# Kernel optimization log

Measured on AMD Instinct MI355X. Metric: run time of the kernel, lower is better.

The kernel has to match this reference:

```python
import jax, jax.numpy as jnp
import numpy as np

F = 256          # in_features
T = 8            # num_fragment_ion_types = 4 types * 2 charges
N_MONO, N_CLEAV, N_FRAG, N_OUT = 150000, 100000, 80000, 40000
D_CLEAV, D_JOIN, D_COMB = 4, 2, 4


def setup_inputs() -> dict:
    key = jax.random.key(0)
    ks = jax.random.split(key, 14)
    s = 0.05
    return {
        "feature": jax.random.normal(ks[0], (N_MONO, F), jnp.float32),
        "Wg_lost": jax.random.normal(ks[1], (F, 1), jnp.float32) * s,
        "Wg_ret": jax.random.normal(ks[2], (F, 1), jnp.float32) * s,
        "W_ih": jax.random.normal(ks[3], (4 * F, 2 * F), jnp.float32) * s,
        "W_hh": jax.random.normal(ks[4], (4 * F, F), jnp.float32) * s,
        "b_ih": jax.random.normal(ks[5], (4 * F,), jnp.float32) * s,
        "b_hh": jax.random.normal(ks[6], (4 * F,), jnp.float32) * s,
        "Wg_frag": jax.random.normal(ks[7], (F, 1), jnp.float32) * s,
        "W_out": jax.random.normal(ks[8], (F, T), jnp.float32) * s,
        "b_out": jnp.zeros((T,), jnp.float32),
        "lost_src": jax.random.randint(ks[9], (N_CLEAV, D_CLEAV), 0, N_MONO),
        "retained_src": jax.random.randint(ks[10], (N_CLEAV, D_CLEAV), 0, N_MONO),
        "join_src": jax.random.randint(ks[11], (N_FRAG, D_JOIN), 0, N_CLEAV),
        "combine_src": jax.random.randint(ks[12], (N_OUT, D_COMB), 0, N_FRAG),
    }


def _attention_sum(h, Wg):
    # h: [N, D, F] mailbox; gate = Linear(F,1,no bias); softmax over neighbor axis
    logits = jnp.einsum('ndf,fo->ndo', h, Wg)          # [N, D, 1]
    a = jax.nn.softmax(logits, axis=1)
    return jnp.sum(a * h, axis=1)                       # [N, F]


def _lstm(x, W_ih, W_hh, b_ih, b_hh):
    # x: [N, L, I]; torch nn.LSTM gate order i,f,g,o; zero initial state
    N = x.shape[0]
    H = W_hh.shape[1]
    def step(carry, xt):
        h, c = carry
        gates = xt @ W_ih.T + h @ W_hh.T + b_ih + b_hh  # [N, 4H]
        i, f, g, o = jnp.split(gates, 4, axis=-1)
        c = jax.nn.sigmoid(f) * c + jax.nn.sigmoid(i) * jnp.tanh(g)
        h = jax.nn.sigmoid(o) * jnp.tanh(c)
        return (h, c), h
    init = (jnp.zeros((N, H), x.dtype), jnp.zeros((N, H), x.dtype))
    _, hs = jax.lax.scan(step, init, jnp.swapaxes(x, 0, 1))
    return jnp.swapaxes(hs, 0, 1)                       # [N, L, H]


def reference(feature, Wg_lost, Wg_ret, W_ih, W_hh, b_ih, b_hh,
              Wg_frag, W_out, b_out,
              lost_src, retained_src, join_src, combine_src):
    h_lost = _attention_sum(feature[lost_src], Wg_lost)        # [N_cleav, F]
    h_ret = _attention_sum(feature[retained_src], Wg_ret)      # [N_cleav, F]
    cleav = jnp.concatenate([h_lost, h_ret], axis=-1)          # [N_cleav, 2F]
    # Fragment pull over 'join' edges: LSTM over neighbor set, then attention sum
    hs = _lstm(cleav[join_src], W_ih, W_hh, b_ih, b_hh)        # [N_frag, D_join, F]
    frag = _attention_sum(hs, Wg_frag)                         # [N_frag, F]
    # Output head: Linear + ReLU
    frag_out = jax.nn.relu(frag @ W_out + b_out)               # [N_frag, T]
    # copy_u_sum over 'combine' edges: scatter-sum of src outputs to dst
    return frag_out[combine_src].sum(axis=1)                   # [N_out, T]
```

## Files before the change

kernel.cpp:

```cpp
#include <hip/hip_runtime.h>

typedef unsigned short u16;
typedef unsigned int u32;
typedef float f32x4 __attribute__((ext_vector_type(4)));
typedef __bf16 bf16x8 __attribute__((ext_vector_type(8)));

#define F 256
#define T_OUT 8
#define N_MONO 150000
#define N_CLEAV 100000
#define N_FRAG 80000
#define N_FRAG_PAD 80128
#define N_OUT 40000
#define M_CLEAV_PAD 100352

static __device__ __forceinline__ u16 f2bf(float f) {
  u32 u = __float_as_uint(f);
  u32 r = (u + 0x7FFFu + ((u >> 16) & 1u)) >> 16;
  return (u16)r;
}
static __device__ __forceinline__ float bf2f(u16 b) {
  return __uint_as_float(((u32)b) << 16);
}
static __device__ __forceinline__ float sigmoidf(float x) {
  return __frcp_rn(1.0f + __expf(-x));
}
static __device__ __forceinline__ float fast_tanh(float x) {
  return 1.0f - 2.0f * __frcp_rn(__expf(2.0f * x) + 1.0f);
}
static __device__ __forceinline__ void async_copy16(const u16* g, const u16* l) {
  __builtin_amdgcn_global_load_lds(
      (const __attribute__((address_space(1))) u32*)g,
      (__attribute__((address_space(3))) u32*)l,
      16, 0, 0);
}

__global__ __launch_bounds__(256) void prep_kernel(
    const float* __restrict__ Wih, const float* __restrict__ Whh,
    const float* __restrict__ bih, const float* __restrict__ bhh,
    u16* __restrict__ Wihb, u16* __restrict__ Whhb, float* __restrict__ bias) {
  int i = blockIdx.x * 256 + threadIdx.x;
  if (i < 1024 * 512) Wihb[i] = f2bf(Wih[i]);
  if (i < 1024 * 256) Whhb[i] = f2bf(Whh[i]);
  if (i < 1024) bias[i] = bih[i] + bhh[i];
}

__global__ __launch_bounds__(256) void feat_prep(
    const float* __restrict__ feat, const float* __restrict__ WgL,
    const float* __restrict__ WgR, u16* __restrict__ featb,
    float* __restrict__ glog) {
  int wave = threadIdx.x >> 6, lane = threadIdx.x & 63;
  int n = blockIdx.x * 4 + wave;
  if (n >= N_MONO) return;
  float4 x = *(const float4*)(feat + (size_t)n * F + lane * 4);
  u32 lo = (u32)f2bf(x.x) | ((u32)f2bf(x.y) << 16);
  u32 hi = (u32)f2bf(x.z) | ((u32)f2bf(x.w) << 16);
  *(uint2*)(featb + (size_t)n * F + lane * 4) = make_uint2(lo, hi);
  float4 wl = *(const float4*)(WgL + lane * 4);
  float4 wr = *(const float4*)(WgR + lane * 4);
  float pl = x.x * wl.x + x.y * wl.y + x.z * wl.z + x.w * wl.w;
  float pr = x.x * wr.x + x.y * wr.y + x.z * wr.z + x.w * wr.w;
#pragma unroll
  for (int off = 32; off; off >>= 1) {
    pl += __shfl_xor(pl, off);
    pr += __shfl_xor(pr, off);
  }
  if (lane == 0) {
    glog[n * 2] = pl;
    glog[n * 2 + 1] = pr;
  }
}

__global__ __launch_bounds__(256) void attn_pull2(
    const u16* __restrict__ featb, const float* __restrict__ glog,
    const int* __restrict__ lostS, const int* __restrict__ retS,
    u16* __restrict__ cleav) {
  int wave = threadIdx.x >> 6, lane = threadIdx.x & 63;
  int n0 = blockIdx.x * 8 + wave * 2;
  if (n0 >= N_CLEAV) return;
  int r[2][2][4];
#pragma unroll
  for (int c = 0; c < 2; ++c) {
    int4 rl = *(const int4*)(lostS + (n0 + c) * 4);
    int4 rr = *(const int4*)(retS + (n0 + c) * 4);
    r[c][0][0] = rl.x; r[c][0][1] = rl.y; r[c][0][2] = rl.z; r[c][0][3] = rl.w;
    r[c][1][0] = rr.x; r[c][1][1] = rr.y; r[c][1][2] = rr.z; r[c][1][3] = rr.w;
  }
  ushort4 x4[2][2][4];
  float lg[2][2][4];
#pragma unroll
  for (int c = 0; c < 2; ++c)
#pragma unroll
    for (int sg = 0; sg < 2; ++sg)
#pragma unroll
      for (int d = 0; d < 4; ++d) {
        x4[c][sg][d] = *(const ushort4*)(featb + (size_t)r[c][sg][d] * F + lane * 4);
        lg[c][sg][d] = glog[r[c][sg][d] * 2 + sg];
      }
#pragma unroll
  for (int c = 0; c < 2; ++c)
#pragma unroll
    for (int sg = 0; sg < 2; ++sg) {
      float l0 = lg[c][sg][0], l1 = lg[c][sg][1];
      float l2 = lg[c][sg][2], l3 = lg[c][sg][3];
      float mx = fmaxf(fmaxf(l0, l1), fmaxf(l2, l3));
      float e0 = __expf(l0 - mx), e1 = __expf(l1 - mx);
      float e2 = __expf(l2 - mx), e3 = __expf(l3 - mx);
      float inv = __frcp_rn(e0 + e1 + e2 + e3);
      float a[4] = {e0 * inv, e1 * inv, e2 * inv, e3 * inv};
      float acc[4] = {0.f, 0.f, 0.f, 0.f};
#pragma unroll
      for (int d = 0; d < 4; ++d) {
        const u16* xp = (const u16*)&x4[c][sg][d];
#pragma unroll
        for (int k = 0; k < 4; k++) acc[k] += a[d] * bf2f(xp[k]);
      }
      u32 lo = (u32)f2bf(acc[0]) | ((u32)f2bf(acc[1]) << 16);
      u32 hi = (u32)f2bf(acc[2]) | ((u32)f2bf(acc[3]) << 16);
      *(uint2*)(cleav + (size_t)(n0 + c) * 512 + sg * 256 + lane * 4) =
          make_uint2(lo, hi);
    }
}

__global__ __launch_bounds__(512, 2) void gemm224(
    const u16* __restrict__ A, const u16* __restrict__ Bw,
    u16* __restrict__ C, const float* __restrict__ bias,
    int nper, int mstrips_valid) {
  constexpr int K = 512, BM = 224;
  constexpr int AREG = BM * 64;
  constexpr int BSZ = AREG + 16384;
  constexpr int WMH = BM / 2;
  constexpr int IB = BM / 32;
  constexpr int IB_HI = IB - 4;
  __shared__ u16 sh[2][BSZ];
  const int flat = blockIdx.x;
  const int xcd = flat & 7;
  const int w = flat >> 3;
  const int mstrip = xcd * nper + (w >> 2);
  const int nstrip = w & 3;
  if (mstrip >= mstrips_valid) return;
  const int m0 = mstrip * BM;
  const int n0 = nstrip * 256;

  const int tid = threadIdx.x;
  const int lane = tid & 63;
  const int wave = tid >> 6;
  const int quad = lane >> 4;
  const int l16 = lane & 15;
  const int s7 = l16 & 7;
  const int wm2 = wave >> 2;
  const int wn4 = wave & 3;

  const int arow = (wm2 * WMH + l16) * 64;
  const int brow = AREG + (wn4 * 64 + l16) * 64;
  const int coff0 = (quad ^ s7) * 8;
  const int coff1 = ((4 + quad) ^ s7) * 8;

  int sr[4], sw[4], dwv[4];
#pragma unroll
  for (int r = 0; r < 4; r++) {
    int c = r * 512 + tid;
    sr[r] = c >> 3;
    sw[r] = ((c & 7) ^ ((c >> 3) & 7)) * 8;
    dwv[r] = (r * 512 + (tid & ~63)) * 8;
  }
  const u16* Abase = A + (size_t)m0 * K;
  const u16* Bbase = Bw + (size_t)n0 * K;

  auto stageA = [&](int buf, int kt, int h) {
#pragma unroll
    for (int rr = 0; rr < 2; rr++) {
      int r = 2 * h + rr;
      if (r * 512 + tid < BM * 8)
        async_copy16(Abase + (size_t)sr[r] * K + kt * 64 + sw[r], &sh[buf][dwv[r]]);
    }
  };
  auto stageB = [&](int buf, int kt, int h) {
#pragma unroll
    for (int rr = 0; rr < 2; rr++) {
      int r = 2 * h + rr;
      async_copy16(Bbase + (size_t)sr[r] * K + kt * 64 + sw[r], &sh[buf][AREG + dwv[r]]);
    }
  };

  f32x4 acc[IB][4];
#pragma unroll
  for (int i = 0; i < IB; i++)
#pragma unroll
    for (int j = 0; j < 4; j++) acc[i][j] = (f32x4){0.f, 0.f, 0.f, 0.f};

  constexpr int nK = K / 64;
  stageA(0, 0, 0); stageA(0, 0, 1); stageB(0, 0, 0); stageB(0, 0, 1);
  stageB(1, 1, 0); stageB(1, 1, 1);
  __builtin_amdgcn_s_waitcnt(0xF74);
  __builtin_amdgcn_s_barrier();

  bf16x8 a[4][2], b0[2][2], b1[2][2];
#pragma unroll
  for (int t = 0; t < nK; ++t) {
    const int bsel = t & 1;
    const u16* S = &sh[bsel][0];

#pragma unroll
    for (int i = 0; i < 4; i++) {
      a[i][0] = *(const bf16x8*)&S[arow + i * 1024 + coff0];
      a[i][1] = *(const bf16x8*)&S[arow + i * 1024 + coff1];
    }
#pragma unroll
    for (int j = 0; j < 2; j++) {
      b0[j][0] = *(const bf16x8*)&S[brow + j * 1024 + coff0];
      b0[j][1] = *(const bf16x8*)&S[brow + j * 1024 + coff1];
    }
    if (t + 1 < nK) stageA(bsel ^ 1, t + 1, 0);
    __builtin_amdgcn_s_waitcnt(0xC87F);
    __builtin_amdgcn_s_barrier();
    __builtin_amdgcn_s_waitcnt(0xC07F);
    __builtin_amdgcn_sched_barrier(0);
    __builtin_amdgcn_s_setprio(1);
#pragma unroll
    for (int i = 0; i < 4; i++)
#pragma unroll
      for (int j = 0; j < 2; j++) {
        acc[i][j] = __builtin_amdgcn_mfma_f32_16x16x32_bf16(a[i][0], b0[j][0], acc[i][j], 0, 0, 0);
        acc[i][j] = __builtin_amdgcn_mfma_f32_16x16x32_bf16(a[i][1], b0[j][1], acc[i][j], 0, 0, 0);
      }
    __builtin_amdgcn_s_setprio(0);
    __builtin_amdgcn_s_barrier();

#pragma unroll
    for (int j = 0; j < 2; j++) {
      b1[j][0] = *(const bf16x8*)&S[brow + (2 + j) * 1024 + coff0];
      b1[j][1] = *(const bf16x8*)&S[brow + (2 + j) * 1024 + coff1];
    }
    if (t + 1 < nK) stageA(bsel ^ 1, t + 1, 1);
    __builtin_amdgcn_s_barrier();
    __builtin_amdgcn_s_waitcnt(0xC07F);
    __builtin_amdgcn_sched_barrier(0);
    __builtin_amdgcn_s_setprio(1);
#pragma unroll
    for (int i = 0; i < 4; i++)
#pragma unroll
      for (int j = 0; j < 2; j++) {
        acc[i][2 + j] = __builtin_amdgcn_mfma_f32_16x16x32_bf16(a[i][0], b1[j][0], acc[i][2 + j], 0, 0, 0);
        acc[i][2 + j] = __builtin_amdgcn_mfma_f32_16x16x32_bf16(a[i][1], b1[j][1], acc[i][2 + j], 0, 0, 0);
      }
    __builtin_amdgcn_s_setprio(0);
    __builtin_amdgcn_s_barrier();

#pragma unroll
    for (int i = 0; i < IB_HI; i++) {
      a[i][0] = *(const bf16x8*)&S[arow + (4 + i) * 1024 + coff0];
      a[i][1] = *(const bf16x8*)&S[arow + (4 + i) * 1024 + coff1];
    }
    if (t + 2 < nK) stageB(bsel, t + 2, 0);
    __builtin_amdgcn_s_barrier();
    __builtin_amdgcn_s_waitcnt(0xC07F);
    __builtin_amdgcn_sched_barrier(0);
    __builtin_amdgcn_s_setprio(1);
#pragma unroll
    for (int i = 0; i < IB_HI; i++)
#pragma unroll
      for (int j = 0; j < 2; j++) {
        acc[4 + i][j] = __builtin_amdgcn_mfma_f32_16x16x32_bf16(a[i][0], b0[j][0], acc[4 + i][j], 0, 0, 0);
        acc[4 + i][j] = __builtin_amdgcn_mfma_f32_16x16x32_bf16(a[i][1], b0[j][1], acc[4 + i][j], 0, 0, 0);
      }
    __builtin_amdgcn_s_setprio(0);
    __builtin_amdgcn_s_barrier();

    if (t + 2 < nK) stageB(bsel, t + 2, 1);
    __builtin_amdgcn_s_barrier();
    __builtin_amdgcn_s_setprio(1);
#pragma unroll
    for (int i = 0; i < IB_HI; i++)
#pragma unroll
      for (int j = 0; j < 2; j++) {
        acc[4 + i][2 + j] = __builtin_amdgcn_mfma_f32_16x16x32_bf16(a[i][0], b1[j][0], acc[4 + i][2 + j], 0, 0, 0);
        acc[4 + i][2 + j] = __builtin_amdgcn_mfma_f32_16x16x32_bf16(a[i][1], b1[j][1], acc[4 + i][2 + j], 0, 0, 0);
      }
    __builtin_amdgcn_s_setprio(0);
    if (t + 2 < nK) __builtin_amdgcn_s_waitcnt(0xF74);
    else            __builtin_amdgcn_s_waitcnt(0xF70);
    __builtin_amdgcn_s_barrier();
  }

  float badd[4];
#pragma unroll
  for (int j = 0; j < 4; j++)
    badd[j] = bias[n0 + wn4 * 64 + j * 16 + l16];
#pragma unroll
  for (int i = 0; i < IB; i++) {
    const int mrow = m0 + wm2 * WMH + i * 16 + quad * 4;
#pragma unroll
    for (int j = 0; j < 4; j++) {
      const int n = n0 + wn4 * 64 + j * 16 + l16;
#pragma unroll
      for (int r = 0; r < 4; r++)
        C[(size_t)(mrow + r) * 1024 + n] = f2bf(acc[i][j][r] + badd[j]);
    }
  }
}

__global__ __launch_bounds__(256) void lstm_step1(
    const u16* __restrict__ P, const int* __restrict__ join,
    u16* __restrict__ h1, u16* __restrict__ c1) {
  int wave = threadIdx.x >> 6, lane = threadIdx.x & 63;
  int m0 = blockIdx.x * 8 + wave * 2;
  if (m0 >= N_FRAG_PAD) return;
#pragma unroll
  for (int c = 0; c < 2; ++c) {
    int m = m0 + c;
    if (m >= N_FRAG) {
      if (m < N_FRAG_PAD) {
        *(ushort4*)(h1 + (size_t)m * 256 + lane * 4) = make_ushort4(0, 0, 0, 0);
        *(ushort4*)(c1 + (size_t)m * 256 + lane * 4) = make_ushort4(0, 0, 0, 0);
      }
    }
  }
  if (m0 + 1 >= N_FRAG) return;
  int j0a = join[2 * m0];
  int j0b = join[2 * (m0 + 1)];
  const u16* rowa = P + (size_t)j0a * 1024 + lane * 4;
  const u16* rowb = P + (size_t)j0b * 1024 + lane * 4;
  ushort4 iva = *(const ushort4*)(rowa);
  ushort4 gva = *(const ushort4*)(rowa + 512);
  ushort4 ova = *(const ushort4*)(rowa + 768);
  ushort4 ivb = *(const ushort4*)(rowb);
  ushort4 gvb = *(const ushort4*)(rowb + 512);
  ushort4 ovb = *(const ushort4*)(rowb + 768);
#pragma unroll
  for (int c = 0; c < 2; ++c) {
    const u16* ivp = (const u16*)(c ? &ivb : &iva);
    const u16* gvp = (const u16*)(c ? &gvb : &gva);
    const u16* ovp = (const u16*)(c ? &ovb : &ova);
    ushort4 h4, c4;
    u16* h4p = (u16*)&h4;
    u16* c4p = (u16*)&c4;
#pragma unroll
    for (int k = 0; k < 4; k++) {
      float cc = sigmoidf(bf2f(ivp[k])) * fast_tanh(bf2f(gvp[k]));
      float hv = sigmoidf(bf2f(ovp[k])) * fast_tanh(cc);
      h4p[k] = f2bf(hv);
      c4p[k] = f2bf(cc);
    }
    *(ushort4*)(h1 + (size_t)(m0 + c) * 256 + lane * 4) = h4;
    *(ushort4*)(c1 + (size_t)(m0 + c) * 256 + lane * 4) = c4;
  }
}

__global__ __launch_bounds__(256, 3) void g2fuse(
    const u16* __restrict__ h1A, const u16* __restrict__ Whhb,
    const u16* __restrict__ P, const int* __restrict__ join,
    const u16* __restrict__ c1in, u16* __restrict__ h2s) {
  constexpr int K = 256;
  __shared__ u16 sh[6][128 * 32];
  const int b = blockIdx.x;
  const int xcd = b & 7;
  const int k = b >> 3;
  const int nstrip = k & 7;
  const int mstrip = (k >> 3) * 8 + xcd;
  if (mstrip >= 626) return;
  const int m0 = mstrip * 128;

  const int tid = threadIdx.x;
  const int lane = tid & 63;
  const int wave = tid >> 6;
  const int quad = lane >> 4;
  const int l16 = lane & 15;
  const int wm = (wave & 1) * 64;
  const int wnq = wave >> 1;
  const int wn = wnq * 64;

  int srow[2], skoff[2], ldsoff[2], brow[2];
#pragma unroll
  for (int jj = 0; jj < 2; jj++) {
    int c = jj * 256 + tid;
    int row = c >> 2;
    srow[jj] = row;
    skoff[jj] = ((c & 3) ^ ((c >> 3) & 3)) * 8;
    ldsoff[jj] = (jj * 256 + (tid & ~63)) * 8;
    brow[jj] = ((row >> 4) & 3) * 256 + nstrip * 32 + ((row >> 6) << 4) + (row & 15);
  }
  const u16* Abase = h1A + (size_t)m0 * K;

  int jrow[8];
#pragma unroll
  for (int rd = 0; rd < 8; rd++) {
    int mm = m0 + rd * 16 + (tid >> 4);
    jrow[rd] = join[2 * (mm < N_FRAG ? mm : N_FRAG - 1) + 1];
  }

  auto stage = [&](int buf, int k0) {
#pragma unroll
    for (int jj = 0; jj < 2; jj++)
      async_copy16(Abase + (size_t)srow[jj] * K + k0 + skoff[jj], &sh[buf][ldsoff[jj]]);
#pragma unroll
    for (int jj = 0; jj < 2; jj++)
      async_copy16(Whhb + (size_t)brow[jj] * K + k0 + skoff[jj], &sh[3 + buf][ldsoff[jj]]);
  };

  f32x4 acc[4][4];
#pragma unroll
  for (int i = 0; i < 4; i++)
#pragma unroll
    for (int j = 0; j < 4; j++) acc[i][j] = (f32x4){0.f, 0.f, 0.f, 0.f};

  constexpr int nK = K / 32;
  stage(0, 0);
  stage(1, 32);
#pragma unroll
  for (int t = 0; t < nK; ++t) {
    if (t < nK - 1) __builtin_amdgcn_s_waitcnt(0xF74);
    else            __builtin_amdgcn_s_waitcnt(0xF70);
    __builtin_amdgcn_s_barrier();
    if (t + 2 < nK) stage((t + 2) % 3, (t + 2) * 32);
    const int buf = t % 3;
    bf16x8 af[4], bfr[4];
#pragma unroll
    for (int i = 0; i < 4; i++) {
      int m = wm + i * 16 + l16;
      int jp = quad ^ ((m >> 1) & 3);
      af[i] = *(const bf16x8*)&sh[buf][m * 32 + jp * 8];
    }
#pragma unroll
    for (int j = 0; j < 4; j++) {
      int n = wn + j * 16 + l16;
      int jp = quad ^ ((n >> 1) & 3);
      bfr[j] = *(const bf16x8*)&sh[3 + buf][n * 32 + jp * 8];
    }
#pragma unroll
    for (int i = 0; i < 4; i++)
#pragma unroll
      for (int j = 0; j < 4; j++)
        acc[i][j] = __builtin_amdgcn_mfma_f32_16x16x32_bf16(af[i], bfr[j], acc[i][j], 0, 0, 0);
  }

  __builtin_amdgcn_s_barrier();
  const int u_ = wnq * 16 + l16;
  u16 c1r[4][4];
#pragma unroll
  for (int i = 0; i < 4; i++)
#pragma unroll
    for (int r = 0; r < 4; r++) {
      int m = m0 + wm + i * 16 + quad * 4 + r;
      c1r[i][r] = c1in[(size_t)m * 256 + nstrip * 32 + u_];
    }
  u16* Pl = &sh[0][0];
  {
    const int g = (tid >> 2) & 3;
    const int chunk = tid & 3;
#pragma unroll
    for (int rd = 0; rd < 8; rd++) {
      const int mloc = rd * 16 + (tid >> 4);
      const int cphys = chunk ^ ((mloc >> 2) & 3);
      async_copy16(P + (size_t)jrow[rd] * 1024 + g * 256 + nstrip * 32 + cphys * 8,
                   &Pl[(size_t)(rd * 256 + (tid & ~63)) * 8]);
    }
  }
  __builtin_amdgcn_s_waitcnt(0xF70);
  __builtin_amdgcn_s_barrier();
  __builtin_amdgcn_sched_barrier(0);

#pragma unroll
  for (int i = 0; i < 4; i++) {
#pragma unroll
    for (int r = 0; r < 4; r++) {
      const int mloc = wm + i * 16 + quad * 4 + r;
      const int m = m0 + mloc;
      const int base = (mloc * 16 + ((u_ >> 3) ^ ((mloc >> 2) & 3))) * 8 + (u_ & 7);
      float gi = acc[i][0][r] + bf2f(Pl[base]);
      float gf = acc[i][1][r] + bf2f(Pl[base + 32]);
      float gg = acc[i][2][r] + bf2f(Pl[base + 64]);
      float go = acc[i][3][r] + bf2f(Pl[base + 96]);
      float c1v = bf2f(c1r[i][r]);
      float cv = sigmoidf(gf) * c1v + sigmoidf(gi) * fast_tanh(gg);
      float hv = sigmoidf(go) * fast_tanh(cv);
      h2s[(size_t)m * 256 + nstrip * 32 + u_] = f2bf(hv);
    }
  }
}

__global__ __launch_bounds__(256) void lstm_attn_out(
    const u16* __restrict__ h1, const u16* __restrict__ h2s,
    const float* __restrict__ Wg, const float* __restrict__ Wout,
    const float* __restrict__ bout, float* __restrict__ frag_out) {
  int wave = threadIdx.x >> 6, lane = threadIdx.x & 63;
  int m0 = blockIdx.x * 8 + wave * 2;
  if (m0 >= N_FRAG) return;
  const int nf = (m0 + 1 < N_FRAG) ? 2 : 1;
  ushort4 h1v[2], h2v[2];
#pragma unroll
  for (int c = 0; c < 2; ++c) {
    int m = m0 + (c < nf ? c : 0);
    h1v[c] = *(const ushort4*)(h1 + (size_t)m * 256 + lane * 4);
    h2v[c] = *(const ushort4*)(h2s + (size_t)m * 256 + lane * 4);
  }
  float4 wg = *(const float4*)(Wg + lane * 4);
  const float* wgp = (const float*)&wg;

  float p1[2], p2[2];
#pragma unroll
  for (int c = 0; c < 2; ++c) {
    const u16* h1p = (const u16*)&h1v[c];
    const u16* h2p = (const u16*)&h2v[c];
    float a = 0.f, b = 0.f;
#pragma unroll
    for (int k = 0; k < 4; k++) {
      a += bf2f(h1p[k]) * wgp[k];
      b += bf2f(h2p[k]) * wgp[k];
    }
    p1[c] = a; p2[c] = b;
  }
#pragma unroll
  for (int off = 32; off; off >>= 1)
#pragma unroll
    for (int c = 0; c < 2; ++c) {
      p1[c] += __shfl_xor(p1[c], off);
      p2[c] += __shfl_xor(p2[c], off);
    }

  float acc[2][8];
#pragma unroll
  for (int c = 0; c < 2; ++c) {
    float mx = fmaxf(p1[c], p2[c]);
    float e1 = __expf(p1[c] - mx), e2 = __expf(p2[c] - mx);
    float inv = __frcp_rn(e1 + e2);
    float a1 = e1 * inv, a2 = e2 * inv;
    const u16* h1p = (const u16*)&h1v[c];
    const u16* h2p = (const u16*)&h2v[c];
#pragma unroll
    for (int t = 0; t < 8; t++) acc[c][t] = 0.f;
#pragma unroll
    for (int k = 0; k < 4; k++) {
      float frag = a1 * bf2f(h1p[k]) + a2 * bf2f(h2p[k]);
      int h = lane * 4 + k;
      float4 w0 = *(const float4*)(Wout + h * 8);
      float4 w1 = *(const float4*)(Wout + h * 8 + 4);
      acc[c][0] += frag * w0.x; acc[c][1] += frag * w0.y;
      acc[c][2] += frag * w0.z; acc[c][3] += frag * w0.w;
      acc[c][4] += frag * w1.x; acc[c][5] += frag * w1.y;
      acc[c][6] += frag * w1.z; acc[c][7] += frag * w1.w;
    }
  }
#pragma unroll
  for (int off = 32; off; off >>= 1)
#pragma unroll
    for (int c = 0; c < 2; ++c)
#pragma unroll
      for (int t = 0; t < 8; t++) acc[c][t] += __shfl_xor(acc[c][t], off);
  if (lane == 0) {
#pragma unroll
    for (int c = 0; c < 2; ++c) {
      if (c >= nf) break;
      float4 o0, o1;
      o0.x = fmaxf(acc[c][0] + bout[0], 0.f);
      o0.y = fmaxf(acc[c][1] + bout[1], 0.f);
      o0.z = fmaxf(acc[c][2] + bout[2], 0.f);
      o0.w = fmaxf(acc[c][3] + bout[3], 0.f);
      o1.x = fmaxf(acc[c][4] + bout[4], 0.f);
      o1.y = fmaxf(acc[c][5] + bout[5], 0.f);
      o1.z = fmaxf(acc[c][6] + bout[6], 0.f);
      o1.w = fmaxf(acc[c][7] + bout[7], 0.f);
      *(float4*)(frag_out + (size_t)(m0 + c) * 8) = o0;
      *(float4*)(frag_out + (size_t)(m0 + c) * 8 + 4) = o1;
    }
  }
}

__global__ __launch_bounds__(256) void scatter_sum(
    const float* __restrict__ frag_out, const int* __restrict__ comb,
    float* __restrict__ out) {
  int tid = blockIdx.x * 256 + threadIdx.x;
  if (tid >= N_OUT * 8) return;
  int n = tid >> 3, t = tid & 7;
  float s = 0.f;
#pragma unroll
  for (int d = 0; d < 4; d++) {
    int f = comb[n * 4 + d];
    s += frag_out[(size_t)f * 8 + t];
  }
  out[tid] = s;
}

extern "C" void kernel_launch(void* const* d_in, const int* in_sizes, int n_in,
                              void* d_out, int out_size, void* d_ws, size_t ws_size,
                              hipStream_t stream) {
  const float* feature = (const float*)d_in[0];
  const float* WgL = (const float*)d_in[1];
  const float* WgR = (const float*)d_in[2];
  const float* Wih = (const float*)d_in[3];
  const float* Whh = (const float*)d_in[4];
  const float* bih = (const float*)d_in[5];
  const float* bhh = (const float*)d_in[6];
  const float* Wgf = (const float*)d_in[7];
  const float* Wout = (const float*)d_in[8];
  const float* bout = (const float*)d_in[9];
  const int* lostS = (const int*)d_in[10];
  const int* retS = (const int*)d_in[11];
  const int* joinS = (const int*)d_in[12];
  const int* combS = (const int*)d_in[13];
  float* out = (float*)d_out;

  char* ws = (char*)d_ws;
  size_t off = 0;
  auto alloc = [&](size_t bytes) -> char* {
    char* p = ws + off;
    off = (off + bytes + 255) & ~(size_t)255;
    return p;
  };
  u16* Wihb = (u16*)alloc((size_t)1024 * 512 * 2);
  u16* Whhb = (u16*)alloc((size_t)1024 * 256 * 2);
  float* bias = (float*)alloc(1024 * 4);
  u16* P = (u16*)alloc((size_t)M_CLEAV_PAD * 1024 * 2);
  u16* h1 = (u16*)alloc((size_t)N_FRAG_PAD * 256 * 2);
  u16* c1 = (u16*)alloc((size_t)N_FRAG_PAD * 256 * 2);
  u16* h2s = (u16*)alloc((size_t)N_FRAG_PAD * 256 * 2);
  float* frag_out = (float*)alloc((size_t)N_FRAG * 8 * 4);
  u16* cleav = (u16*)alloc((size_t)M_CLEAV_PAD * 512 * 2);
  u16* featb = P;
  float* glog = (float*)(P + (size_t)N_MONO * F);

  prep_kernel<<<2048, 256, 0, stream>>>(Wih, Whh, bih, bhh, Wihb, Whhb, bias);
  feat_prep<<<(N_MONO + 3) / 4, 256, 0, stream>>>(feature, WgL, WgR, featb, glog);
  attn_pull2<<<N_CLEAV / 8, 256, 0, stream>>>(featb, glog, lostS, retS, cleav);
  gemm224<<<1792, 512, 0, stream>>>(cleav, Wihb, P, bias, 56, 448);
  lstm_step1<<<N_FRAG_PAD / 8, 256, 0, stream>>>(P, joinS, h1, c1);
  g2fuse<<<632 * 8, 256, 0, stream>>>(h1, Whhb, P, joinS, c1, h2s);
  lstm_attn_out<<<(N_FRAG + 7) / 8, 256, 0, stream>>>(
      h1, h2s, Wgf, Wout, bout, frag_out);
  scatter_sum<<<(N_OUT * 8 + 255) / 256, 256, 0, stream>>>(frag_out, combS, out);
}
```

Baseline: 634.3 us.

## Make gemm224 persistent over seven M-strips with continuous cross-tile pipelining

The GEMM launch drops from 1792 blocks, one output tile each, to 256 persistent blocks. Each block walks 7 consecutive M-strips for one N-strip, so the async-copy double-buffer pipeline keeps running across tile boundaries. Accumulators are written out and reset after every 8 K-steps. This is meant to remove per-tile prologue and epilogue stalls and block launch overhead. In exchange it leaves fewer blocks for load balancing, drops the full unroll of the K loop, and puts the bf16 store epilogue inside the main loop, where it is not overlapped with compute.

```diff
diff --git a/kernel.cpp b/kernel.cpp
--- a/kernel.cpp
+++ b/kernel.cpp
@@ -124,22 +124,22 @@
 
 __global__ __launch_bounds__(512, 2) void gemm224(
     const u16* __restrict__ A, const u16* __restrict__ Bw,
-    u16* __restrict__ C, const float* __restrict__ bias,
-    int nper, int mstrips_valid) {
+    u16* __restrict__ C, const float* __restrict__ bias) {
   constexpr int K = 512, BM = 224;
   constexpr int AREG = BM * 64;
   constexpr int BSZ = AREG + 16384;
   constexpr int WMH = BM / 2;
   constexpr int IB = BM / 32;
   constexpr int IB_HI = IB - 4;
+  constexpr int NT = 7;
+  constexpr int G = NT * 8;
   __shared__ u16 sh[2][BSZ];
-  const int flat = blockIdx.x;
-  const int xcd = flat & 7;
-  const int w = flat >> 3;
-  const int mstrip = xcd * nper + (w >> 2);
-  const int nstrip = w & 3;
-  if (mstrip >= mstrips_valid) return;
-  const int m0 = mstrip * BM;
+  const int b = blockIdx.x;
+  const int xcd = b & 7;
+  const int s = b >> 3;
+  const int nstrip = s & 3;
+  const int mgrp = s >> 2;
+  const int mstrip0 = xcd * 56 + mgrp * 7;
   const int n0 = nstrip * 256;
 
   const int tid = threadIdx.x;
@@ -164,18 +164,20 @@
     sw[r] = ((c & 7) ^ ((c >> 3) & 7)) * 8;
     dwv[r] = (r * 512 + (tid & ~63)) * 8;
   }
-  const u16* Abase = A + (size_t)m0 * K;
   const u16* Bbase = Bw + (size_t)n0 * K;
 
-  auto stageA = [&](int buf, int kt, int h) {
+  auto stageA = [&](int buf, int g, int h) {
+    const u16* Ab = A + (size_t)(mstrip0 + (g >> 3)) * BM * K;
+    const int kt = g & 7;
 #pragma unroll
     for (int rr = 0; rr < 2; rr++) {
       int r = 2 * h + rr;
       if (r * 512 + tid < BM * 8)
-        async_copy16(Abase + (size_t)sr[r] * K + kt * 64 + sw[r], &sh[buf][dwv[r]]);
+        async_copy16(Ab + (size_t)sr[r] * K + kt * 64 + sw[r], &sh[buf][dwv[r]]);
     }
   };
-  auto stageB = [&](int buf, int kt, int h) {
+  auto stageB = [&](int buf, int g, int h) {
+    const int kt = g & 7;
 #pragma unroll
     for (int rr = 0; rr < 2; rr++) {
       int r = 2 * h + rr;
@@ -183,22 +185,25 @@
     }
   };
 
+  float badd[4];
+#pragma unroll
+  for (int j = 0; j < 4; j++)
+    badd[j] = bias[n0 + wn4 * 64 + j * 16 + l16];
+
   f32x4 acc[IB][4];
 #pragma unroll
   for (int i = 0; i < IB; i++)
 #pragma unroll
     for (int j = 0; j < 4; j++) acc[i][j] = (f32x4){0.f, 0.f, 0.f, 0.f};
 
-  constexpr int nK = K / 64;
   stageA(0, 0, 0); stageA(0, 0, 1); stageB(0, 0, 0); stageB(0, 0, 1);
   stageB(1, 1, 0); stageB(1, 1, 1);
   __builtin_amdgcn_s_waitcnt(0xF74);
   __builtin_amdgcn_s_barrier();
 
   bf16x8 a[4][2], b0[2][2], b1[2][2];
-#pragma unroll
-  for (int t = 0; t < nK; ++t) {
-    const int bsel = t & 1;
+  for (int g = 0; g < G; ++g) {
+    const int bsel = g & 1;
     const u16* S = &sh[bsel][0];
 
 #pragma unroll
@@ -211,7 +216,7 @@
       b0[j][0] = *(const bf16x8*)&S[brow + j * 1024 + coff0];
       b0[j][1] = *(const bf16x8*)&S[brow + j * 1024 + coff1];
     }
-    if (t + 1 < nK) stageA(bsel ^ 1, t + 1, 0);
+    if (g + 1 < G) stageA(bsel ^ 1, g + 1, 0);
     __builtin_amdgcn_s_waitcnt(0xC87F);
     __builtin_amdgcn_s_barrier();
     __builtin_amdgcn_s_waitcnt(0xC07F);
@@ -232,7 +237,7 @@
       b1[j][0] = *(const bf16x8*)&S[brow + (2 + j) * 1024 + coff0];
       b1[j][1] = *(const bf16x8*)&S[brow + (2 + j) * 1024 + coff1];
     }
-    if (t + 1 < nK) stageA(bsel ^ 1, t + 1, 1);
+    if (g + 1 < G) stageA(bsel ^ 1, g + 1, 1);
     __builtin_amdgcn_s_barrier();
     __builtin_amdgcn_s_waitcnt(0xC07F);
     __builtin_amdgcn_sched_barrier(0);
@@ -252,7 +257,7 @@
       a[i][0] = *(const bf16x8*)&S[arow + (4 + i) * 1024 + coff0];
       a[i][1] = *(const bf16x8*)&S[arow + (4 + i) * 1024 + coff1];
     }
-    if (t + 2 < nK) stageB(bsel, t + 2, 0);
+    if (g + 2 < G) stageB(bsel, g + 2, 0);
     __builtin_amdgcn_s_barrier();
     __builtin_amdgcn_s_waitcnt(0xC07F);
     __builtin_amdgcn_sched_barrier(0);
@@ -267,7 +272,7 @@
     __builtin_amdgcn_s_setprio(0);
     __builtin_amdgcn_s_barrier();
 
-    if (t + 2 < nK) stageB(bsel, t + 2, 1);
+    if (g + 2 < G) stageB(bsel, g + 2, 1);
     __builtin_amdgcn_s_barrier();
     __builtin_amdgcn_s_setprio(1);
 #pragma unroll
@@ -278,24 +283,27 @@
         acc[4 + i][2 + j] = __builtin_amdgcn_mfma_f32_16x16x32_bf16(a[i][1], b1[j][1], acc[4 + i][2 + j], 0, 0, 0);
       }
     __builtin_amdgcn_s_setprio(0);
-    if (t + 2 < nK) __builtin_amdgcn_s_waitcnt(0xF74);
-    else            __builtin_amdgcn_s_waitcnt(0xF70);
-    __builtin_amdgcn_s_barrier();
-  }
-
-  float badd[4];
-#pragma unroll
-  for (int j = 0; j < 4; j++)
-    badd[j] = bias[n0 + wn4 * 64 + j * 16 + l16];
-#pragma unroll
-  for (int i = 0; i < IB; i++) {
-    const int mrow = m0 + wm2 * WMH + i * 16 + quad * 4;
-#pragma unroll
-    for (int j = 0; j < 4; j++) {
-      const int n = n0 + wn4 * 64 + j * 16 + l16;
-#pragma unroll
-      for (int r = 0; r < 4; r++)
-        C[(size_t)(mrow + r) * 1024 + n] = f2bf(acc[i][j][r] + badd[j]);
+    if (g + 2 < G) __builtin_amdgcn_s_waitcnt(0xF74);
+    else           __builtin_amdgcn_s_waitcnt(0xF70);
+    __builtin_amdgcn_s_barrier();
+
+    if ((g & 7) == 7) {
+      const int m0 = (mstrip0 + (g >> 3)) * BM;
+#pragma unroll
+      for (int i = 0; i < IB; i++) {
+        const int mrow = m0 + wm2 * WMH + i * 16 + quad * 4;
+#pragma unroll
+        for (int j = 0; j < 4; j++) {
+          const int n = n0 + wn4 * 64 + j * 16 + l16;
+#pragma unroll
+          for (int r = 0; r < 4; r++)
+            C[(size_t)(mrow + r) * 1024 + n] = f2bf(acc[i][j][r] + badd[j]);
+        }
+      }
+#pragma unroll
+      for (int i = 0; i < IB; i++)
+#pragma unroll
+        for (int j = 0; j < 4; j++) acc[i][j] = (f32x4){0.f, 0.f, 0.f, 0.f};
     }
   }
 }
@@ -622,7 +630,7 @@
   prep_kernel<<<2048, 256, 0, stream>>>(Wih, Whh, bih, bhh, Wihb, Whhb, bias);
   feat_prep<<<(N_MONO + 3) / 4, 256, 0, stream>>>(feature, WgL, WgR, featb, glog);
   attn_pull2<<<N_CLEAV / 8, 256, 0, stream>>>(featb, glog, lostS, retS, cleav);
-  gemm224<<<1792, 512, 0, stream>>>(cleav, Wihb, P, bias, 56, 448);
+  gemm224<<<256, 512, 0, stream>>>(cleav, Wihb, P, bias);
   lstm_step1<<<N_FRAG_PAD / 8, 256, 0, stream>>>(P, joinS, h1, c1);
   g2fuse<<<632 * 8, 256, 0, stream>>>(h1, Whhb, P, joinS, c1, h2s);
   lstm_attn_out<<<(N_FRAG + 7) / 8, 256, 0, stream>>>(
```

After: 652.5 us. 1.03x slower.
